# Kernel tuning notes

Measured on AMD Instinct MI355X. Metric: run time of the kernel, lower is better.

## Reference

```python
import jax, jax.numpy as jnp
import numpy as np

K = 5          # involution kernel size
GC = 8         # group_channels
EPS = 1e-5     # BatchNorm eps


def _unfold(x, k):
    """torch nn.Unfold(k, dilation=1, padding=(k-1)//2, stride=1) equivalent.
    x: [B,C,H,W] -> [B, C, k*k, H, W] with channel-major ordering matching
    torch's view(b, groups, group_channels, k*k, h, w)."""
    p = (k - 1) // 2
    B, C, H, W = x.shape
    xp = jnp.pad(x, ((0, 0), (0, 0), (p, p), (p, p)))
    # fixed small loop over k*k taps (k=5 -> 25 slices)
    taps = [xp[:, :, i:i + H, j:j + W] for i in range(k) for j in range(k)]
    return jnp.stack(taps, axis=2)  # [B, C, k*k, H, W]


def involution_fwd(x, w1, b1, bn_gamma, bn_beta, bn_mean, bn_var, w2, b2):
    B, C, H, W = x.shape
    groups = C // GC
    # conv1: 1x1 conv + BN(eval) + ReLU6
    y = jnp.einsum('bchw,oc->bohw', x, w1) + b1[None, :, None, None]
    scale = bn_gamma / jnp.sqrt(bn_var + EPS)
    y = y * scale[None, :, None, None] + (bn_beta - bn_mean * scale)[None, :, None, None]
    y = jnp.clip(y, 0.0, 6.0)
    # conv2: 1x1 conv -> per-pixel kernels [B, k*k*groups, H, W]
    kern = jnp.einsum('bchw,oc->bohw', y, w2) + b2[None, :, None, None]
    kern = kern.reshape(B, groups, 1, K * K, H, W)  # broadcast over group_channels
    # unfold + weighted sum over k*k taps
    patches = _unfold(x, K).reshape(B, groups, GC, K * K, H, W)
    out = (kern * patches).sum(axis=3).reshape(B, C, H, W)
    return out


def setup_inputs() -> dict:
    key = jax.random.key(0)
    ks = jax.random.split(key, 9)
    B, C, H, W = 8, 256, 64, 64
    cr = C // 4                       # reduction_ratio = 4
    groups = C // GC                  # 32
    return {
        'x': jax.random.normal(ks[0], (B, C, H, W), jnp.float32),
        'w1': jax.random.normal(ks[1], (cr, C), jnp.float32) * 0.05,
        'b1': jax.random.normal(ks[2], (cr,), jnp.float32) * 0.05,
        'bn_gamma': jax.random.uniform(ks[3], (cr,), jnp.float32, 0.5, 1.5),
        'bn_beta': jax.random.normal(ks[4], (cr,), jnp.float32) * 0.05,
        'bn_mean': jax.random.normal(ks[5], (cr,), jnp.float32) * 0.05,
        'bn_var': jax.random.uniform(ks[6], (cr,), jnp.float32, 0.5, 1.5),
        'w2': jax.random.normal(ks[7], (K * K * groups, cr), jnp.float32) * 0.05,
        'b2': jax.random.normal(ks[8], (K * K * groups,), jnp.float32) * 0.05,
    }


def reference(x, w1, b1, bn_gamma, bn_beta, bn_mean, bn_var, w2, b2):
    return involution_fwd(x, w1, b1, bn_gamma, bn_beta, bn_mean, bn_var, w2, b2)
```

## Files before the change

kernel.cpp:

```cpp
#include <hip/hip_runtime.h>

#define BB   8
#define CC   256
#define HH   64
#define WW   64
#define CR   64
#define NG   32
#define GC   8
#define KK   25
#define HW   (HH*WW)

typedef __attribute__((ext_vector_type(8))) short short8;
typedef __attribute__((ext_vector_type(4))) float f32x4;

__device__ __forceinline__ unsigned short f2bf(float f) {
    unsigned u = __builtin_bit_cast(unsigned, f);
    u += 0x7FFFu + ((u >> 16) & 1u);
    return (unsigned short)(u >> 16);
}

__global__ __launch_bounds__(256) void prep_kernel(
    const float* __restrict__ w1, const float* __restrict__ b1,
    const float* __restrict__ gamma, const float* __restrict__ beta,
    const float* __restrict__ mean, const float* __restrict__ var,
    const float* __restrict__ w2,
    unsigned short* __restrict__ w1a, float* __restrict__ b1f,
    unsigned short* __restrict__ w2p)
{
    int gid = blockIdx.x;
    if (gid < 256) {
        int idx = gid * 256 + threadIdx.x;
        int j  = idx & 7;
        int l  = (idx >> 3) & 63;
        int ki = (idx >> 9) & 1;
        int nt = (idx >> 10) & 1;
        int g  = idx >> 11;
        int nl = nt * 16 + (l & 15);
        int k  = ki * 32 + (l >> 4) * 8 + j;
        float v = (nl < KK) ? w2[(g * KK + nl) * CR + k] : 0.0f;
        w2p[idx] = f2bf(v);
    } else {
        int idx = (gid - 256) * 256 + threadIdx.x;
        int j  = idx & 7;
        int l  = (idx >> 3) & 63;
        int mt = (idx >> 9) & 3;
        int ki = (idx >> 11) & 7;
        int r  = mt * 16 + (l & 15);
        int c  = ki * 32 + (l >> 4) * 8 + j;
        float scale = gamma[r] * rsqrtf(var[r] + 1e-5f);
        w1a[idx] = f2bf(w1[r * CC + c] * scale);
        if (idx < CR) {
            float s = gamma[idx] * rsqrtf(var[idx] + 1e-5f);
            b1f[idx] = (b1[idx] - mean[idx]) * s + beta[idx];
        }
    }
}

__global__ __launch_bounds__(256) void conv1_kernel(
    const float* __restrict__ x, const unsigned short* __restrict__ w1a,
    const float* __restrict__ b1f, unsigned short* __restrict__ ybf)
{
    const int tid  = threadIdx.x;
    const int h    = blockIdx.x;
    const int b    = blockIdx.y;
    const int lane = tid & 63;
    const int wv   = tid >> 6;
    const int l15  = lane & 15;
    const int q    = lane >> 4;
    const int px   = wv * 16 + l15;

    const float*  xc   = x + (size_t)b * CC * HW + h * WW + px;
    const short8* w1a8 = (const short8*)w1a;

    f32x4 cfr[4];
    #pragma unroll
    for (int mt = 0; mt < 4; ++mt) cfr[mt] = (f32x4){0.f, 0.f, 0.f, 0.f};

    #pragma unroll
    for (int ki = 0; ki < 8; ++ki) {
        short8 bfr;
        #pragma unroll
        for (int j = 0; j < 8; ++j) {
            float v = xc[(ki * 32 + q * 8 + j) * HW];
            bfr[j] = (short)f2bf(v);
        }
        #pragma unroll
        for (int mt = 0; mt < 4; ++mt) {
            short8 afr = w1a8[(ki * 4 + mt) * 64 + lane];
            cfr[mt] = __builtin_amdgcn_mfma_f32_16x16x32_bf16(afr, bfr, cfr[mt], 0, 0, 0);
        }
    }

    unsigned short* yb = ybf + ((size_t)(b * HH + h) * WW + px) * CR;
    #pragma unroll
    for (int mt = 0; mt < 4; ++mt) {
        unsigned pk[2];
        #pragma unroll
        for (int rp = 0; rp < 2; ++rp) {
            float v0 = cfr[mt][rp * 2 + 0] + b1f[mt * 16 + q * 4 + rp * 2 + 0];
            float v1 = cfr[mt][rp * 2 + 1] + b1f[mt * 16 + q * 4 + rp * 2 + 1];
            v0 = fminf(fmaxf(v0, 0.0f), 6.0f);
            v1 = fminf(fmaxf(v1, 0.0f), 6.0f);
            pk[rp] = (unsigned)f2bf(v0) | ((unsigned)f2bf(v1) << 16);
        }
        *(uint2*)(yb + mt * 16 + q * 4) = make_uint2(pk[0], pk[1]);
    }
}

__global__ __launch_bounds__(256, 4) void invol_kernel(
    const float* __restrict__ x, const unsigned short* __restrict__ ybf,
    const unsigned short* __restrict__ w2p, const float* __restrict__ b2,
    float* __restrict__ out)
{
    __shared__ float klds[4][32 * 65];

    const int tid  = threadIdx.x;
    const int h    = blockIdx.x;
    const int b    = blockIdx.y;
    const int gq   = blockIdx.z;
    const int lane = tid & 63;
    const int wv   = __builtin_amdgcn_readfirstlane(tid >> 6);
    float* kw = klds[wv];

    const int l15 = lane & 15;
    const int q   = lane >> 4;

    short8 afr[4][2];
    const unsigned short* yb = ybf + (size_t)(b * HH + h) * WW * CR;
    #pragma unroll
    for (int mt = 0; mt < 4; ++mt)
        #pragma unroll
        for (int ki = 0; ki < 2; ++ki)
            afr[mt][ki] = *(const short8*)(yb + (mt * 16 + l15) * CR + ki * 32 + q * 8);

    bool val[5];
    #pragma unroll
    for (int dj = 0; dj < 5; ++dj) {
        int ww  = lane + dj - 2;
        val[dj] = (ww >= 0) && (ww < WW);
    }

    const short8* w2p8 = (const short8*)w2p;

    #pragma unroll 1
    for (int gl = 0; gl < 4; ++gl) {
        const int g = gq * 16 + wv * 4 + gl;

        f32x4 cfr[4][2];
        #pragma unroll
        for (int nt = 0; nt < 2; ++nt) {
            int nl = nt * 16 + l15;
            float vb = b2[g * KK + min(nl, KK - 1)];
            vb = (nl < KK) ? vb : 0.0f;
            #pragma unroll
            for (int mt = 0; mt < 4; ++mt)
                cfr[mt][nt] = (f32x4){vb, vb, vb, vb};
        }

        #pragma unroll
        for (int nt = 0; nt < 2; ++nt) {
            short8 bf0 = w2p8[((g * 2 + nt) * 2 + 0) * 64 + lane];
            short8 bf1 = w2p8[((g * 2 + nt) * 2 + 1) * 64 + lane];
            #pragma unroll
            for (int mt = 0; mt < 4; ++mt) {
                cfr[mt][nt] = __builtin_amdgcn_mfma_f32_16x16x32_bf16(
                    afr[mt][0], bf0, cfr[mt][nt], 0, 0, 0);
                cfr[mt][nt] = __builtin_amdgcn_mfma_f32_16x16x32_bf16(
                    afr[mt][1], bf1, cfr[mt][nt], 0, 0, 0);
            }
        }

        #pragma unroll
        for (int mt = 0; mt < 4; ++mt)
            #pragma unroll
            for (int nt = 0; nt < 2; ++nt) {
                int n  = nt * 16 + l15;
                int px = mt * 16 + q * 4;
                #pragma unroll
                for (int r = 0; r < 4; ++r)
                    kw[n * 65 + px + r] = cfr[mt][nt][r];
            }

        float oacc[GC];
        #pragma unroll
        for (int j = 0; j < GC; ++j) oacc[j] = 0.0f;

        const float* xg = x + (size_t)(b * CC + g * GC) * HW;
        #pragma unroll
        for (int di = 0; di < 5; ++di) {
            int hh = h + di - 2;
            if (hh >= 0 && hh < HH) {
                float ks[5];
                #pragma unroll
                for (int dj = 0; dj < 5; ++dj) {
                    float kv = kw[(di * 5 + dj) * 65 + lane];
                    ks[dj] = val[dj] ? kv : 0.0f;
                }
                #pragma unroll
                for (int j = 0; j < GC; ++j) {
                    float xv  = xg[(j * HH + hh) * WW + lane];
                    float xm2 = __shfl(xv, lane - 2, 64);
                    float xm1 = __shfl(xv, lane - 1, 64);
                    float xp1 = __shfl(xv, lane + 1, 64);
                    float xp2 = __shfl(xv, lane + 2, 64);
                    oacc[j] = fmaf(ks[0], xm2, oacc[j]);
                    oacc[j] = fmaf(ks[1], xm1, oacc[j]);
                    oacc[j] = fmaf(ks[2], xv,  oacc[j]);
                    oacc[j] = fmaf(ks[3], xp1, oacc[j]);
                    oacc[j] = fmaf(ks[4], xp2, oacc[j]);
                }
            }
        }

        float* oc = out + ((size_t)(b * CC + g * GC) * HH + h) * WW + lane;
        #pragma unroll
        for (int j = 0; j < GC; ++j) oc[j * HW] = oacc[j];
    }
}

extern "C" void kernel_launch(void* const* d_in, const int* in_sizes, int n_in,
                              void* d_out, int out_size, void* d_ws, size_t ws_size,
                              hipStream_t stream) {
    const float* x     = (const float*)d_in[0];
    const float* w1    = (const float*)d_in[1];
    const float* b1    = (const float*)d_in[2];
    const float* gamma = (const float*)d_in[3];
    const float* beta  = (const float*)d_in[4];
    const float* mean  = (const float*)d_in[5];
    const float* var   = (const float*)d_in[6];
    const float* w2    = (const float*)d_in[7];
    const float* b2    = (const float*)d_in[8];
    float* out = (float*)d_out;

    char* ws = (char*)d_ws;
    unsigned short* w1a = (unsigned short*)ws;
    float*          b1f = (float*)(ws + 32768);
    unsigned short* w2p = (unsigned short*)(ws + 33024);
    unsigned short* ybf = (unsigned short*)(ws + 164096);

    prep_kernel<<<320, 256, 0, stream>>>(w1, b1, gamma, beta, mean, var, w2,
                                         w1a, b1f, w2p);
    conv1_kernel<<<dim3(HH, BB), 256, 0, stream>>>(x, w1a, b1f, ybf);
    invol_kernel<<<dim3(HH, BB, 2), 256, 0, stream>>>(x, ybf, w2p, b2, out);
}
```

Baseline: 135.5 us.

## Restructure involution kernel to per-group waves with register row window

The involution kernel now gives each wave one group over four output rows. Lanes are remapped to (8-pixel width chunk × channel), and the x rows the taps need are kept in a sliding register window loaded with vector loads. This replaces the per-tap wave shuffles, avoids re-reading the same x rows for adjacent output rows, and uses float4 LDS and global accesses. In exchange, every wave re-reads its row's ybf fragments and recomputes the conv2 MFMA for its own group. Global stores are now scattered across eight channel planes per wave instead of one contiguous row.

Measured after the change: 143.9 us. 1.06x slower.

```diff
diff --git a/kernel.cpp b/kernel.cpp
--- a/kernel.cpp
+++ b/kernel.cpp
@@ -112,110 +112,121 @@
     const unsigned short* __restrict__ w2p, const float* __restrict__ b2,
     float* __restrict__ out)
 {
-    __shared__ float klds[4][32 * 65];
+    __shared__ float klds[4][32 * 68];
 
     const int tid  = threadIdx.x;
-    const int h    = blockIdx.x;
+    const int bx   = blockIdx.x;
+    const int hq   = bx >> 3;
+    const int gs   = bx & 7;
     const int b    = blockIdx.y;
-    const int gq   = blockIdx.z;
     const int lane = tid & 63;
     const int wv   = __builtin_amdgcn_readfirstlane(tid >> 6);
+    const int g    = gs * 4 + wv;
+    const int h0   = hq * 4;
+    const int wq   = lane >> 3;
+    const int ch   = lane & 7;
+    const int w0   = wq * 8;
+    const int l15  = lane & 15;
+    const int q    = lane >> 4;
     float* kw = klds[wv];
 
-    const int l15 = lane & 15;
-    const int q   = lane >> 4;
-
-    short8 afr[4][2];
-    const unsigned short* yb = ybf + (size_t)(b * HH + h) * WW * CR;
-    #pragma unroll
-    for (int mt = 0; mt < 4; ++mt)
+    const short8* w2p8 = (const short8*)w2p;
+    short8 bf[2][2];
+    #pragma unroll
+    for (int nt = 0; nt < 2; ++nt)
         #pragma unroll
         for (int ki = 0; ki < 2; ++ki)
-            afr[mt][ki] = *(const short8*)(yb + (mt * 16 + l15) * CR + ki * 32 + q * 8);
-
-    bool val[5];
-    #pragma unroll
-    for (int dj = 0; dj < 5; ++dj) {
-        int ww  = lane + dj - 2;
-        val[dj] = (ww >= 0) && (ww < WW);
-    }
-
-    const short8* w2p8 = (const short8*)w2p;
-
-    #pragma unroll 1
-    for (int gl = 0; gl < 4; ++gl) {
-        const int g = gq * 16 + wv * 4 + gl;
-
+            bf[nt][ki] = w2p8[((g * 2 + nt) * 2 + ki) * 64 + lane];
+    float b2v[2];
+    #pragma unroll
+    for (int nt = 0; nt < 2; ++nt) {
+        int t = nt * 16 + l15;
+        b2v[nt] = b2[g * KK + min(t, KK - 1)];
+    }
+
+    float xw[8][12];
+    const float* xch = x + (size_t)(b * CC + g * GC + ch) * HW;
+    const bool wlo = (wq == 0), whi = (wq == 7);
+
+    #define LOADROW(ridx_)                                                     \
+    {                                                                          \
+        int hh = h0 - 2 + (ridx_);                                             \
+        int hc = min(max(hh, 0), HH - 1);                                      \
+        const float* xr = xch + hc * WW;                                       \
+        float2 elo = *(const float2*)(xr + max(w0 - 2, 0));                    \
+        float4 m0  = *(const float4*)(xr + w0);                                \
+        float4 m1  = *(const float4*)(xr + w0 + 4);                            \
+        float2 ehi = *(const float2*)(xr + min(w0 + 8, WW - 2));               \
+        xw[ridx_][0]  = wlo ? 0.0f : elo.x;                                    \
+        xw[ridx_][1]  = wlo ? 0.0f : elo.y;                                    \
+        xw[ridx_][2]  = m0.x; xw[ridx_][3] = m0.y;                             \
+        xw[ridx_][4]  = m0.z; xw[ridx_][5] = m0.w;                             \
+        xw[ridx_][6]  = m1.x; xw[ridx_][7] = m1.y;                             \
+        xw[ridx_][8]  = m1.z; xw[ridx_][9] = m1.w;                             \
+        xw[ridx_][10] = whi ? 0.0f : ehi.x;                                    \
+        xw[ridx_][11] = whi ? 0.0f : ehi.y;                                    \
+    }
+
+    LOADROW(0) LOADROW(1) LOADROW(2) LOADROW(3) LOADROW(4)
+
+    #pragma unroll
+    for (int ho = 0; ho < 4; ++ho) {
+        const int h = h0 + ho;
+
+        const unsigned short* yb = ybf + (size_t)(b * HH + h) * WW * CR;
         f32x4 cfr[4][2];
         #pragma unroll
-        for (int nt = 0; nt < 2; ++nt) {
-            int nl = nt * 16 + l15;
-            float vb = b2[g * KK + min(nl, KK - 1)];
-            vb = (nl < KK) ? vb : 0.0f;
+        for (int mt = 0; mt < 4; ++mt)
             #pragma unroll
-            for (int mt = 0; mt < 4; ++mt)
-                cfr[mt][nt] = (f32x4){vb, vb, vb, vb};
-        }
-
-        #pragma unroll
-        for (int nt = 0; nt < 2; ++nt) {
-            short8 bf0 = w2p8[((g * 2 + nt) * 2 + 0) * 64 + lane];
-            short8 bf1 = w2p8[((g * 2 + nt) * 2 + 1) * 64 + lane];
+            for (int nt = 0; nt < 2; ++nt)
+                cfr[mt][nt] = (f32x4){b2v[nt], b2v[nt], b2v[nt], b2v[nt]};
+        #pragma unroll
+        for (int ki = 0; ki < 2; ++ki)
             #pragma unroll
             for (int mt = 0; mt < 4; ++mt) {
-                cfr[mt][nt] = __builtin_amdgcn_mfma_f32_16x16x32_bf16(
-                    afr[mt][0], bf0, cfr[mt][nt], 0, 0, 0);
-                cfr[mt][nt] = __builtin_amdgcn_mfma_f32_16x16x32_bf16(
-                    afr[mt][1], bf1, cfr[mt][nt], 0, 0, 0);
+                short8 afr = *(const short8*)(yb + (mt * 16 + l15) * CR + ki * 32 + q * 8);
+                #pragma unroll
+                for (int nt = 0; nt < 2; ++nt)
+                    cfr[mt][nt] = __builtin_amdgcn_mfma_f32_16x16x32_bf16(
+                        afr, bf[nt][ki], cfr[mt][nt], 0, 0, 0);
             }
-        }
-
         #pragma unroll
         for (int mt = 0; mt < 4; ++mt)
             #pragma unroll
-            for (int nt = 0; nt < 2; ++nt) {
-                int n  = nt * 16 + l15;
-                int px = mt * 16 + q * 4;
-                #pragma unroll
-                for (int r = 0; r < 4; ++r)
-                    kw[n * 65 + px + r] = cfr[mt][nt][r];
-            }
-
-        float oacc[GC];
-        #pragma unroll
-        for (int j = 0; j < GC; ++j) oacc[j] = 0.0f;
-
-        const float* xg = x + (size_t)(b * CC + g * GC) * HW;
+            for (int nt = 0; nt < 2; ++nt)
+                *(float4*)(&kw[(nt * 16 + l15) * 68 + mt * 16 + q * 4]) =
+                    (float4){cfr[mt][nt][0], cfr[mt][nt][1], cfr[mt][nt][2], cfr[mt][nt][3]};
+
+        float oacc[8];
+        #pragma unroll
+        for (int i = 0; i < 8; ++i) oacc[i] = 0.0f;
+
         #pragma unroll
         for (int di = 0; di < 5; ++di) {
             int hh = h + di - 2;
             if (hh >= 0 && hh < HH) {
-                float ks[5];
                 #pragma unroll
                 for (int dj = 0; dj < 5; ++dj) {
-                    float kv = kw[(di * 5 + dj) * 65 + lane];
-                    ks[dj] = val[dj] ? kv : 0.0f;
-                }
-                #pragma unroll
-                for (int j = 0; j < GC; ++j) {
-                    float xv  = xg[(j * HH + hh) * WW + lane];
-                    float xm2 = __shfl(xv, lane - 2, 64);
-                    float xm1 = __shfl(xv, lane - 1, 64);
-                    float xp1 = __shfl(xv, lane + 1, 64);
-                    float xp2 = __shfl(xv, lane + 2, 64);
-                    oacc[j] = fmaf(ks[0], xm2, oacc[j]);
-                    oacc[j] = fmaf(ks[1], xm1, oacc[j]);
-                    oacc[j] = fmaf(ks[2], xv,  oacc[j]);
-                    oacc[j] = fmaf(ks[3], xp1, oacc[j]);
-                    oacc[j] = fmaf(ks[4], xp2, oacc[j]);
+                    float4 k0 = *(const float4*)(&kw[(di * 5 + dj) * 68 + w0]);
+                    float4 k1 = *(const float4*)(&kw[(di * 5 + dj) * 68 + w0 + 4]);
+                    #pragma unroll
+                    for (int wi = 0; wi < 4; ++wi) {
+                        oacc[wi]     = fmaf(k0[wi], xw[ho + di][wi + dj],     oacc[wi]);
+                        oacc[wi + 4] = fmaf(k1[wi], xw[ho + di][wi + 4 + dj], oacc[wi + 4]);
+                    }
                 }
             }
         }
 
-        float* oc = out + ((size_t)(b * CC + g * GC) * HH + h) * WW + lane;
-        #pragma unroll
-        for (int j = 0; j < GC; ++j) oc[j * HW] = oacc[j];
-    }
+        float* op = out + ((size_t)(b * CC + g * GC + ch) * HH + h) * WW + w0;
+        *(float4*)op       = (float4){oacc[0], oacc[1], oacc[2], oacc[3]};
+        *(float4*)(op + 4) = (float4){oacc[4], oacc[5], oacc[6], oacc[7]};
+
+        if (ho == 0) LOADROW(5)
+        if (ho == 1) LOADROW(6)
+        if (ho == 2) LOADROW(7)
+    }
+    #undef LOADROW
 }
 
 extern "C" void kernel_launch(void* const* d_in, const int* in_sizes, int n_in,
@@ -241,5 +252,5 @@
     prep_kernel<<<320, 256, 0, stream>>>(w1, b1, gamma, beta, mean, var, w2,
                                          w1a, b1f, w2p);
     conv1_kernel<<<dim3(HH, BB), 256, 0, stream>>>(x, w1a, b1f, ybf);
-    invol_kernel<<<dim3(HH, BB, 2), 256, 0, stream>>>(x, ybf, w2p, b2, out);
-}
+    invol_kernel<<<dim3(128, BB), 256, 0, stream>>>(x, ybf, w2p, b2, out);
+}
```
